# Performance work log

Measured on AMD Instinct MI355X. Metric: run time of the kernel, lower is better.

The kernel has to match this reference:

```python
import jax, jax.numpy as jnp
import numpy as np

# module constants (from init_kwargs)
CS, NV, ED = 8, 4, 32          # codebook_size, num_variables, embedding_dim
VIEWS, D, KSZ = 3, 16, 3        # num_input_channels, depth, kernel_size
HW = 14                         # 7 * scale (scale=2)
CSP = 8                         # spatial of conv_shape after three valid 3x3 convs: 14->12->10->8
KSTATES = CS ** NV              # 4096 combinatorial discrete states


def _elu(x):
    return jnp.where(x > 0, x, jnp.expm1(x))


def _conv_t(x, w, b):
    # PyTorch ConvTranspose2d(stride=1, padding=0); w: (Cin, Cout, k, k)
    wf = jnp.flip(w, (2, 3)).transpose(1, 0, 2, 3)  # -> (Cout, Cin, k, k)
    p = w.shape[2] - 1
    y = jax.lax.conv_general_dilated(x, wf, (1, 1), [(p, p), (p, p)],
                                     dimension_numbers=('NCHW', 'OIHW', 'NCHW'))
    return y + b[None, :, None, None]


def setup_inputs() -> dict:
    key = jax.random.key(0)
    ks = jax.random.split(key, 10)
    rn = lambda k, shape, s=1.0: jax.random.normal(k, shape, jnp.float32) * s
    return {
        'x': rn(ks[0], (64, VIEWS, HW, HW)),
        'latent_embedding': rn(ks[1], (NV, CS, ED)),
        'lin_w': rn(ks[2], (VIEWS, ED * NV, 4 * D * CSP * CSP), 0.05),
        'lin_b': rn(ks[3], (VIEWS, 4 * D * CSP * CSP), 0.05),
        'w1': rn(ks[4], (VIEWS, 4 * D, 2 * D, KSZ, KSZ), 0.05),
        'b1': rn(ks[5], (VIEWS, 2 * D), 0.05),
        'w2': rn(ks[6], (VIEWS, 2 * D, D, KSZ, KSZ), 0.05),
        'b2': rn(ks[7], (VIEWS, D), 0.05),
        'w3': rn(ks[8], (VIEWS, D, 1, KSZ, KSZ), 0.05),
        'b3': rn(ks[9], (VIEWS, 1), 0.05),
    }


def reference(x, latent_embedding, lin_w, lin_b, w1, b1, w2, b2, w3, b3):
    # all combinations of codebook indices (itertools.product order): [K, NV]
    all_idcs = jnp.stack(
        jnp.meshgrid(*([jnp.arange(CS)] * NV), indexing='ij'), -1).reshape(-1, NV)
    # gather: z[k, v, :] = latent_embedding[v, all_idcs[k, v], :]
    z = latent_embedding[jnp.arange(NV)[None, :], all_idcs]       # [K, NV, ED]
    zf = z.reshape(KSTATES, NV * ED)                              # 'b n d -> b (n d)'

    def decode(lw, lb, W1, B1, W2, B2, W3, B3):
        h = (zf @ lw + lb).reshape(KSTATES, 4 * D, CSP, CSP)
        h = _elu(_conv_t(h, W1, B1))
        h = _elu(_conv_t(h, W2, B2))
        h = _conv_t(h, W3, B3)
        return h[:, 0]                                            # [K, HW, HW]

    m = jax.vmap(decode)(lin_w, lin_b, w1, b1, w2, b2, w3, b3)    # [views, K, HW, HW]
    m = jnp.transpose(m, (1, 0, 2, 3))                            # [K, views, HW, HW]

    # obs_logits = -0.5 * sum_{h,w} (m[None] - x[:, None])**2, computed without
    # materializing the [B, K, views, HW, HW] broadcast tensor
    m2 = jnp.sum(m * m, axis=(-2, -1))                            # [K, views]
    x2 = jnp.sum(x * x, axis=(-2, -1))                            # [B, views]
    cross = jnp.einsum('kvhw,bvhw->bkv', m, x)                    # [B, K, views]
    return -0.5 * (m2[None] + x2[:, None] - 2.0 * cross)          # [B, K, views]
```

## Files before the change

### kernel.cpp

```cpp
#include <hip/hip_runtime.h>
#include <cstddef>


typedef __attribute__((ext_vector_type(4))) float f32x4;
typedef _Float16 half8v __attribute__((ext_vector_type(8)));
typedef _Float16 half4v __attribute__((ext_vector_type(4)));
typedef _Float16 half2v __attribute__((ext_vector_type(2)));

static __device__ __forceinline__ float elu(float s) {
    float e = __expf(s) - 1.0f;
    return s > 0.f ? s : e;
}
static __device__ __forceinline__ float dot2acc(int hpair, int wpair, float acc) {
#if __has_builtin(__builtin_amdgcn_fdot2)
    return __builtin_amdgcn_fdot2(__builtin_bit_cast(half2v, hpair),
                                  __builtin_bit_cast(half2v, wpair), acc, false);
#else
    half2v h = __builtin_bit_cast(half2v, hpair);
    half2v w = __builtin_bit_cast(half2v, wpair);
    acc = fmaf((float)h.x, (float)w.x, acc);
    return fmaf((float)h.y, (float)w.y, acc);
#endif
}
static __device__ __forceinline__ int sh2addr(int c, int r) {
    return c * 392 + r * 24 + (((r >> 2) & 3) << 3);
}

__global__ __launch_bounds__(320) void prep_kernel(const float* __restrict__ x,
                                                   const float* __restrict__ le,
                                                   const float* __restrict__ lin_w,
                                                   const float* __restrict__ lin_b,
                                                   const float* __restrict__ w1,
                                                   const float* __restrict__ b1,
                                                   const float* __restrict__ w2,
                                                   float* __restrict__ Qa,
                                                   float* __restrict__ Qb,
                                                   float* __restrict__ x2,
                                                   short* __restrict__ xB,
                                                   short* __restrict__ Wf) {
    int bid = blockIdx.x;
    int t = threadIdx.x;
    if (bid >= 198) {
        int pid = bid - 198;
        int v = pid % 3, part = pid / 3;
        if (part < 4) {
            int nb = part;
            short* xBv = xB + v * 14336 + nb * 3584;
            for (int idx = t; idx < 3584; idx += 320) {
                int j = idx & 7, lane = (idx >> 3) & 63, s = idx >> 9;
                int px = s * 32 + ((lane >> 4) << 3) + j;
                int b  = nb * 16 + (lane & 15);
                float val = (px < 196) ? x[(b * 3 + v) * 196 + px] : 0.f;
                _Float16 h = (_Float16)val;
                xBv[idx] = __builtin_bit_cast(short, h);
            }
        } else if (part == 4) {
            int w = t >> 6, lane = t & 63;
            for (int b = w; b < 64; b += 5) {
                const float* xp = x + (b * 3 + v) * 196;
                float s = 0.f;
                for (int px = lane; px < 196; px += 64) s = fmaf(xp[px], xp[px], s);
#pragma unroll
                for (int off = 32; off; off >>= 1) s += __shfl_down(s, off, 64);
                if (lane == 0) x2[v * 64 + b] = s;
            }
        } else if (t < 64) {
            int lane = t;
            const float* w2v = w2 + v * 32 * 16 * 9;
            int co = lane & 15;
            int cibase = (lane >> 4) * 8;
#pragma unroll
            for (int tap = 0; tap < 9; ++tap)
#pragma unroll
                for (int j = 0; j < 8; ++j) {
                    _Float16 h = (_Float16)w2v[((cibase + j) * 16 + co) * 9 + tap];
                    Wf[(((v * 9 + tap) * 64 + lane) << 3) + j] = __builtin_bit_cast(short, h);
                }
        }
        return;
    }
    __shared__ float sPt[64 * 144];
    __shared__ float sW[16 * 32 * 9];
    int row = bid % 33;
    int v   = (bid / 33) % 3;
    int z   = bid / 99;

    float pacc[16];
    if (t < 256) {
        if (row < 32) {
            int vp = row >> 3;
            const float* base0 = lin_w + (size_t)v * 524288 + (size_t)vp * 32 * 4096 + t;
            const float* lep = le + row * 32;
#pragma unroll
            for (int j = 0; j < 16; ++j) pacc[j] = 0.f;
            for (int e = 0; e < 32; ++e) {
                float lv = lep[e];
                const float* bp = base0 + e * 4096;
#pragma unroll
                for (int j = 0; j < 16; ++j)
                    pacc[j] = fmaf(lv, bp[j * 256], pacc[j]);
            }
        } else {
            const float* bp = lin_b + v * 4096 + t;
#pragma unroll
            for (int j = 0; j < 16; ++j) pacc[j] = bp[j * 256];
        }
    }
    float4* zp = (float4*)sPt;
    for (int i = t; i < 2304; i += 320) zp[i] = float4{0.f, 0.f, 0.f, 0.f};
    __syncthreads();
    if (t < 256) {
#pragma unroll
        for (int j = 0; j < 16; ++j) {
            int i = t + j * 256;
            int ci = i >> 6, r = i & 63, y = r >> 3, xx = r & 7;
            sPt[ci * 144 + (xx + 2) * 12 + (y + 2)] = pacc[j];
        }
    }
    const float* w1v = w1 + (size_t)v * 64 * 32 * 9;
    int co = t / 10, ox = t % 10;
    float acc[10];
#pragma unroll
    for (int i = 0; i < 10; ++i) acc[i] = 0.f;

    for (int c0 = z * 2; c0 < z * 2 + 2; ++c0) {
        __syncthreads();
        for (int i = t; i < 4608; i += 320) sW[i] = w1v[c0 * 4608 + i];
        __syncthreads();
#pragma unroll 2
        for (int ci = 0; ci < 16; ++ci) {
            const float* xp = sPt + (c0 * 16 + ci) * 144;
            const float* wp = sW + (ci * 32 + co) * 9;
            float wv[9];
#pragma unroll
            for (int j = 0; j < 9; ++j) wv[j] = wp[j];
#pragma unroll
            for (int b = 0; b < 3; ++b) {
                const float* colp = xp + (ox + 2 - b) * 12;
                float4 c0v = *(const float4*)(colp);
                float4 c1v = *(const float4*)(colp + 4);
                float4 c2v = *(const float4*)(colp + 8);
                float cv[12] = {c0v.x, c0v.y, c0v.z, c0v.w,
                                c1v.x, c1v.y, c1v.z, c1v.w,
                                c2v.x, c2v.y, c2v.z, c2v.w};
#pragma unroll
                for (int a = 0; a < 3; ++a) {
                    float wgt = wv[a * 3 + b];
#pragma unroll
                    for (int oy = 0; oy < 10; ++oy)
                        acc[oy] = fmaf(cv[oy + 2 - a], wgt, acc[oy]);
                }
            }
        }
    }
    float bb = (z == 0 && row == 32) ? b1[v * 32 + co] : 0.f;
    float* dst = (z == 0 ? Qa : Qb) + (size_t)v * 105600 + row * 3200;
#pragma unroll
    for (int oy = 0; oy < 10; ++oy)
        dst[(ox * 10 + oy) * 32 + co] = acc[oy] + bb;
}

__global__ __launch_bounds__(256) void pair_kernel(const float* __restrict__ Qa,
                                                   const float* __restrict__ Qb,
                                                   float* __restrict__ Q01,
                                                   float* __restrict__ Q23b) {
    int p = blockIdx.x;
    int half = blockIdx.y;
    int v = blockIdx.z;
    const float4* basea = (const float4*)(Qa + (size_t)v * 105600);
    const float4* baseb = (const float4*)(Qb + (size_t)v * 105600);
    if (half == 0) {
        const float4* ra = basea + (p >> 3) * 800;
        const float4* rb = baseb + (p >> 3) * 800;
        const float4* rc = basea + (8 + (p & 7)) * 800;
        const float4* rd = baseb + (8 + (p & 7)) * 800;
        float4* dst = (float4*)(Q01 + (size_t)v * 204800 + p * 3200);
        for (int i = threadIdx.x; i < 800; i += 256) {
            float4 a = ra[i], b = rb[i], c = rc[i], d = rd[i];
            dst[i] = float4{a.x + b.x + c.x + d.x, a.y + b.y + c.y + d.y,
                            a.z + b.z + c.z + d.z, a.w + b.w + c.w + d.w};
        }
    } else {
        const float4* ra = basea + (16 + (p >> 3)) * 800;
        const float4* rb = baseb + (16 + (p >> 3)) * 800;
        const float4* rc = basea + (24 + (p & 7)) * 800;
        const float4* rd = baseb + (24 + (p & 7)) * 800;
        const float4* re = basea + 32 * 800;
        const float4* rf = baseb + 32 * 800;
        float4* dst = (float4*)(Q23b + (size_t)v * 204800 + p * 3200);
        for (int i = threadIdx.x; i < 800; i += 256) {
            float4 a = ra[i], b = rb[i], c = rc[i], d = rd[i], e = re[i], f = rf[i];
            dst[i] = float4{a.x + b.x + c.x + d.x + e.x + f.x,
                            a.y + b.y + c.y + d.y + e.y + f.y,
                            a.z + b.z + c.z + d.z + e.z + f.z,
                            a.w + b.w + c.w + d.w + e.w + f.w};
        }
    }
}

__global__ __launch_bounds__(256) void fused_kernel(const float* __restrict__ Q01,
                                                    const float* __restrict__ Q23b,
                                                    const short* __restrict__ Wf,
                                                    const float* __restrict__ b2,
                                                    const float* __restrict__ w3,
                                                    const float* __restrict__ b3,
                                                    short* __restrict__ Mh,
                                                    float* __restrict__ m2g) {
    __shared__ alignas(16) short sH1[196 * 40];
    __shared__ alignas(16) short sH2[6280];
    __shared__ int sW3p[72];
    __shared__ float sM2;
    int k = blockIdx.x;
    int v = blockIdx.y;
    int t = threadIdx.x;
    int lane = t & 63;
    int g = lane >> 4;

    half8v bfrag[9];
#pragma unroll
    for (int tap = 0; tap < 9; ++tap)
        bfrag[tap] = *(const half8v*)(const void*)(Wf + (((v * 9 + tap) * 64 + lane) << 3));
    float bias2 = b2[v * 16 + (lane & 15)];

    if (t == 0) sM2 = 0.f;
    for (int pix = t; pix < 196; pix += 256) {
        int c = pix / 14, r = pix % 14;
        if (c < 2 || c >= 12 || r < 2 || r >= 12) {
            int4* z = (int4*)(sH1 + pix * 40);
            z[0] = int4{0,0,0,0}; z[1] = int4{0,0,0,0};
            z[2] = int4{0,0,0,0}; z[3] = int4{0,0,0,0};
        }
    }
    {
        int pix = t;
        int c = pix >> 4, r = pix & 15;
        if (c < 2 || c >= 14 || r < 2 || r >= 14) {
            int4* z = (int4*)(sH2 + sh2addr(c, r));
            z[0] = int4{0,0,0,0}; z[1] = int4{0,0,0,0};
        }
    }
    if (t < 72) {
        int tap = t / 8, j = t % 8;
        half2v p = {(_Float16)w3[v * 144 + (2 * j) * 9 + tap],
                    (_Float16)w3[v * 144 + (2 * j + 1) * 9 + tap]};
        sW3p[t] = __builtin_bit_cast(int, p);
    }

    {
        const float4* qa = (const float4*)(Q01  + ((size_t)v * 64 + (k >> 6)) * 3200);
        const float4* qb = (const float4*)(Q23b + ((size_t)v * 64 + (k & 63)) * 3200);
        int ci4 = (t & 7) * 4;
        int pix = t >> 3;
        int cx = pix / 10, ry = pix % 10;
        for (int i = t; i < 800; i += 256) {
            float4 a = qa[i], b = qb[i];
            half4v o = {(_Float16)elu(a.x + b.x), (_Float16)elu(a.y + b.y),
                        (_Float16)elu(a.z + b.z), (_Float16)elu(a.w + b.w)};
            *(half4v*)(void*)(sH1 + ((cx + 2) * 14 + (ry + 2)) * 40 + ci4) = o;
            cx += 3; ry += 2;
            if (ry >= 10) { ry -= 10; ++cx; }
        }
    }
    __syncthreads();

    {
        int w = t >> 6;
        for (int tile = w; tile < 9; tile += 4) {
            int m = tile * 16 + (lane & 15);
            int cx2 = m / 12, ry2 = m % 12;
            const short* basemin = sH1 + (cx2 * 14 + ry2) * 40 + g * 8;
            f32x4 acc0 = {bias2, bias2, bias2, bias2};
            f32x4 acc1 = {0.f, 0.f, 0.f, 0.f};
#pragma unroll
            for (int a = 0; a < 3; ++a)
#pragma unroll
                for (int b = 0; b < 3; ++b) {
                    half8v af = *(const half8v*)(const void*)(basemin + ((2 - b) * 14 + (2 - a)) * 40);
                    int idx = a * 3 + b;
                    if (idx & 1)
                        acc1 = __builtin_amdgcn_mfma_f32_16x16x32_f16(af, bfrag[idx], acc1, 0, 0, 0);
                    else
                        acc0 = __builtin_amdgcn_mfma_f32_16x16x32_f16(af, bfrag[idx], acc0, 0, 0, 0);
                }
            int p0 = tile * 16 + g * 4;
            int cxp = p0 / 12, ryp = p0 % 12;
            int co = lane & 15;
#pragma unroll
            for (int r = 0; r < 4; ++r) {
                _Float16 h = (_Float16)elu(acc0[r] + acc1[r]);
                sH2[sh2addr(cxp + 2, ryp + 2) + co] = __builtin_bit_cast(short, h);
                ++ryp; if (ryp == 12) { ryp = 0; ++cxp; }
            }
        }
    }
    __syncthreads();

    {
        float mval = 0.f;
        if (t < 196) {
            float bias3 = b3[v];
            int ry3 = t / 14, cx3 = t % 14;
            float a0 = bias3, a1 = 0.f, a2 = 0.f, a3 = 0.f;
#pragma unroll
            for (int a = 0; a < 3; ++a)
#pragma unroll
                for (int b = 0; b < 3; ++b) {
                    const short* base = sH2 + sh2addr(cx3 + 2 - b, ry3 + 2 - a);
                    int4 lo = *(const int4*)(const void*)(base);
                    int4 hi = *(const int4*)(const void*)(base + 8);
                    const int* wp = sW3p + (a * 3 + b) * 8;
                    a0 = dot2acc(lo.x, wp[0], a0);
                    a1 = dot2acc(lo.y, wp[1], a1);
                    a2 = dot2acc(lo.z, wp[2], a2);
                    a3 = dot2acc(lo.w, wp[3], a3);
                    a0 = dot2acc(hi.x, wp[4], a0);
                    a1 = dot2acc(hi.y, wp[5], a1);
                    a2 = dot2acc(hi.z, wp[6], a2);
                    a3 = dot2acc(hi.w, wp[7], a3);
                }
            mval = (a0 + a1) + (a2 + a3);
        }
        if (t < 224) {
            _Float16 h = (_Float16)mval;
            Mh[((size_t)v * 4096 + k) * 224 + t] = __builtin_bit_cast(short, h);
        }
        float sq = mval * mval;
#pragma unroll
        for (int off = 32; off; off >>= 1) sq += __shfl_down(sq, off, 64);
        if (lane == 0) atomicAdd(&sM2, sq);
        __syncthreads();
        if (t == 0) m2g[(size_t)v * 4096 + k] = sM2;
    }
}

__global__ __launch_bounds__(256) void gemm_final_kernel(const short* __restrict__ Mh,
                                                         const short* __restrict__ xB,
                                                         const float* __restrict__ m2g,
                                                         const float* __restrict__ x2g,
                                                         float* __restrict__ out) {
    __shared__ float sC[3 * 64 * 17];
    __shared__ float sM2t[48];
    int t = threadIdx.x, lane = t & 63, nb = t >> 6;
    int k0 = blockIdx.x * 16;
    if (t < 48) {
        int v = t % 3, kk = t / 3;
        sM2t[kk * 3 + v] = m2g[(size_t)v * 4096 + k0 + kk];
    }
    int mrow = lane & 15;
    int g = lane >> 4;
#pragma unroll
    for (int v = 0; v < 3; ++v) {
        f32x4 acc = {0.f, 0.f, 0.f, 0.f};
        const short* abase = Mh + ((size_t)v * 4096 + k0 + mrow) * 224 + g * 8;
        const short* bbase = xB + (((v * 4 + nb) * 7) * 64 + lane) * 8;
#pragma unroll
        for (int s = 0; s < 7; ++s) {
            half8v af = *(const half8v*)(const void*)(abase + s * 32);
            half8v bf = *(const half8v*)(const void*)(bbase + s * 512);
            acc = __builtin_amdgcn_mfma_f32_16x16x32_f16(af, bf, acc, 0, 0, 0);
        }
        int b = nb * 16 + mrow;
#pragma unroll
        for (int r = 0; r < 4; ++r)
            sC[(v * 64 + b) * 17 + g * 4 + r] = acc[r];
    }
    __syncthreads();
    int b = t >> 2, q = t & 3;
    float x2v0 = x2g[b], x2v1 = x2g[64 + b], x2v2 = x2g[128 + b];
    float buf[12];
#pragma unroll
    for (int i = 0; i < 4; ++i) {
        int kk = q * 4 + i;
        buf[i * 3 + 0] = sC[(0 * 64 + b) * 17 + kk] - 0.5f * (sM2t[kk * 3 + 0] + x2v0);
        buf[i * 3 + 1] = sC[(1 * 64 + b) * 17 + kk] - 0.5f * (sM2t[kk * 3 + 1] + x2v1);
        buf[i * 3 + 2] = sC[(2 * 64 + b) * 17 + kk] - 0.5f * (sM2t[kk * 3 + 2] + x2v2);
    }
    float* dst = out + ((size_t)b * 4096 + k0) * 3 + q * 12;
    *(float4*)(dst)     = float4{buf[0], buf[1], buf[2],  buf[3]};
    *(float4*)(dst + 4) = float4{buf[4], buf[5], buf[6],  buf[7]};
    *(float4*)(dst + 8) = float4{buf[8], buf[9], buf[10], buf[11]};
}

extern "C" void kernel_launch(void* const* d_in, const int* in_sizes, int n_in,
                              void* d_out, int out_size, void* d_ws, size_t ws_size,
                              hipStream_t stream) {
    const float* x     = (const float*)d_in[0];
    const float* le    = (const float*)d_in[1];
    const float* lin_w = (const float*)d_in[2];
    const float* lin_b = (const float*)d_in[3];
    const float* w1    = (const float*)d_in[4];
    const float* b1    = (const float*)d_in[5];
    const float* w2    = (const float*)d_in[6];
    const float* b2    = (const float*)d_in[7];
    const float* w3    = (const float*)d_in[8];
    const float* b3    = (const float*)d_in[9];
    float* out = (float*)d_out;

    float* ws = (float*)d_ws;
    float* x2g  = ws;
    short* xB   = (short*)(ws + 192);
    short* Wf   = (short*)(ws + 21760);
    float* Qa   = ws + 28736;
    float* Qb   = ws + 345536;
    float* Q01  = ws + 662336;
    float* Q23b = ws + 1276736;
    short* Mh   = (short*)(ws + 1891136);
    float* m2g  = ws + 3267392;

    prep_kernel<<<216, 320, 0, stream>>>(x, le, lin_w, lin_b, w1, b1, w2,
                                         Qa, Qb, x2g, xB, Wf);
    pair_kernel<<<dim3(64, 2, 3), 256, 0, stream>>>(Qa, Qb, Q01, Q23b);
    fused_kernel<<<dim3(4096, 3), 256, 0, stream>>>(Q01, Q23b, Wf, b2, w3, b3, Mh, m2g);
    gemm_final_kernel<<<256, 256, 0, stream>>>(Mh, xB, m2g, x2g, out);
}
```

Before: 180.6 us.

## Drop pair kernel, merge conv1 partials via atomics, process two states per block

Removes the pair-sum kernel. The two z-halves of the first transposed conv now accumulate into one Q buffer with atomicAdd after a memset. The fused kernel handles two codebook states per block: it sums the three shared per-variable partials once, adds the fourth per state, and keeps two H2 buffers. The lin_w and w1 loads also become float4-vectorized. This trades an extra kernel and its intermediate buffers for atomics, a memset, more LDS per block, and half as many blocks.

```diff
diff --git a/kernel.cpp b/kernel.cpp
--- a/kernel.cpp
+++ b/kernel.cpp
@@ -33,8 +33,7 @@
                                                    const float* __restrict__ w1,
                                                    const float* __restrict__ b1,
                                                    const float* __restrict__ w2,
-                                                   float* __restrict__ Qa,
-                                                   float* __restrict__ Qb,
+                                                   float* __restrict__ Q,
                                                    float* __restrict__ x2,
                                                    short* __restrict__ xB,
                                                    short* __restrict__ Wf) {
@@ -85,39 +84,52 @@
     int v   = (bid / 33) % 3;
     int z   = bid / 99;
 
-    float pacc[16];
+    float pj[16];
     if (t < 256) {
         if (row < 32) {
             int vp = row >> 3;
-            const float* base0 = lin_w + (size_t)v * 524288 + (size_t)vp * 32 * 4096 + t;
+            const float* base0 = lin_w + (size_t)v * 524288 + (size_t)vp * 131072 + t * 16;
             const float* lep = le + row * 32;
-#pragma unroll
-            for (int j = 0; j < 16; ++j) pacc[j] = 0.f;
+            f32x4 a0 = {0,0,0,0}, a1 = {0,0,0,0}, a2 = {0,0,0,0}, a3 = {0,0,0,0};
             for (int e = 0; e < 32; ++e) {
                 float lv = lep[e];
-                const float* bp = base0 + e * 4096;
-#pragma unroll
-                for (int j = 0; j < 16; ++j)
-                    pacc[j] = fmaf(lv, bp[j * 256], pacc[j]);
+                const float4* bp = (const float4*)(base0 + e * 4096);
+                float4 b0 = bp[0], b1v_ = bp[1], b2v_ = bp[2], b3v_ = bp[3];
+                a0[0] = fmaf(lv, b0.x, a0[0]);  a0[1] = fmaf(lv, b0.y, a0[1]);
+                a0[2] = fmaf(lv, b0.z, a0[2]);  a0[3] = fmaf(lv, b0.w, a0[3]);
+                a1[0] = fmaf(lv, b1v_.x, a1[0]); a1[1] = fmaf(lv, b1v_.y, a1[1]);
+                a1[2] = fmaf(lv, b1v_.z, a1[2]); a1[3] = fmaf(lv, b1v_.w, a1[3]);
+                a2[0] = fmaf(lv, b2v_.x, a2[0]); a2[1] = fmaf(lv, b2v_.y, a2[1]);
+                a2[2] = fmaf(lv, b2v_.z, a2[2]); a2[3] = fmaf(lv, b2v_.w, a2[3]);
+                a3[0] = fmaf(lv, b3v_.x, a3[0]); a3[1] = fmaf(lv, b3v_.y, a3[1]);
+                a3[2] = fmaf(lv, b3v_.z, a3[2]); a3[3] = fmaf(lv, b3v_.w, a3[3]);
+            }
+#pragma unroll
+            for (int j = 0; j < 4; ++j) {
+                pj[j] = a0[j]; pj[4 + j] = a1[j]; pj[8 + j] = a2[j]; pj[12 + j] = a3[j];
             }
         } else {
-            const float* bp = lin_b + v * 4096 + t;
-#pragma unroll
-            for (int j = 0; j < 16; ++j) pacc[j] = bp[j * 256];
+            const float4* bp = (const float4*)(lin_b + v * 4096 + t * 16);
+#pragma unroll
+            for (int j = 0; j < 4; ++j) {
+                float4 b = bp[j];
+                pj[4 * j] = b.x; pj[4 * j + 1] = b.y; pj[4 * j + 2] = b.z; pj[4 * j + 3] = b.w;
+            }
         }
     }
     float4* zp = (float4*)sPt;
     for (int i = t; i < 2304; i += 320) zp[i] = float4{0.f, 0.f, 0.f, 0.f};
     __syncthreads();
     if (t < 256) {
+        int ci = t >> 2;
 #pragma unroll
         for (int j = 0; j < 16; ++j) {
-            int i = t + j * 256;
-            int ci = i >> 6, r = i & 63, y = r >> 3, xx = r & 7;
-            sPt[ci * 144 + (xx + 2) * 12 + (y + 2)] = pacc[j];
-        }
-    }
-    const float* w1v = w1 + (size_t)v * 64 * 32 * 9;
+            int r = (t & 3) * 16 + j;
+            int y = r >> 3, xx = r & 7;
+            sPt[ci * 144 + (xx + 2) * 12 + (y + 2)] = pj[j];
+        }
+    }
+    const float* w1v = w1 + (size_t)v * 18432;
     int co = t / 10, ox = t % 10;
     float acc[10];
 #pragma unroll
@@ -125,7 +137,8 @@
 
     for (int c0 = z * 2; c0 < z * 2 + 2; ++c0) {
         __syncthreads();
-        for (int i = t; i < 4608; i += 320) sW[i] = w1v[c0 * 4608 + i];
+        const float4* wsrc = (const float4*)(w1v + c0 * 4608);
+        for (int i = t; i < 1152; i += 320) ((float4*)sW)[i] = wsrc[i];
         __syncthreads();
 #pragma unroll 2
         for (int ci = 0; ci < 16; ++ci) {
@@ -154,64 +167,29 @@
         }
     }
     float bb = (z == 0 && row == 32) ? b1[v * 32 + co] : 0.f;
-    float* dst = (z == 0 ? Qa : Qb) + (size_t)v * 105600 + row * 3200;
+    float* dst = Q + (size_t)v * 105600 + row * 3200;
 #pragma unroll
     for (int oy = 0; oy < 10; ++oy)
-        dst[(ox * 10 + oy) * 32 + co] = acc[oy] + bb;
-}
-
-__global__ __launch_bounds__(256) void pair_kernel(const float* __restrict__ Qa,
-                                                   const float* __restrict__ Qb,
-                                                   float* __restrict__ Q01,
-                                                   float* __restrict__ Q23b) {
-    int p = blockIdx.x;
-    int half = blockIdx.y;
-    int v = blockIdx.z;
-    const float4* basea = (const float4*)(Qa + (size_t)v * 105600);
-    const float4* baseb = (const float4*)(Qb + (size_t)v * 105600);
-    if (half == 0) {
-        const float4* ra = basea + (p >> 3) * 800;
-        const float4* rb = baseb + (p >> 3) * 800;
-        const float4* rc = basea + (8 + (p & 7)) * 800;
-        const float4* rd = baseb + (8 + (p & 7)) * 800;
-        float4* dst = (float4*)(Q01 + (size_t)v * 204800 + p * 3200);
-        for (int i = threadIdx.x; i < 800; i += 256) {
-            float4 a = ra[i], b = rb[i], c = rc[i], d = rd[i];
-            dst[i] = float4{a.x + b.x + c.x + d.x, a.y + b.y + c.y + d.y,
-                            a.z + b.z + c.z + d.z, a.w + b.w + c.w + d.w};
-        }
-    } else {
-        const float4* ra = basea + (16 + (p >> 3)) * 800;
-        const float4* rb = baseb + (16 + (p >> 3)) * 800;
-        const float4* rc = basea + (24 + (p & 7)) * 800;
-        const float4* rd = baseb + (24 + (p & 7)) * 800;
-        const float4* re = basea + 32 * 800;
-        const float4* rf = baseb + 32 * 800;
-        float4* dst = (float4*)(Q23b + (size_t)v * 204800 + p * 3200);
-        for (int i = threadIdx.x; i < 800; i += 256) {
-            float4 a = ra[i], b = rb[i], c = rc[i], d = rd[i], e = re[i], f = rf[i];
-            dst[i] = float4{a.x + b.x + c.x + d.x + e.x + f.x,
-                            a.y + b.y + c.y + d.y + e.y + f.y,
-                            a.z + b.z + c.z + d.z + e.z + f.z,
-                            a.w + b.w + c.w + d.w + e.w + f.w};
-        }
-    }
-}
-
-__global__ __launch_bounds__(256) void fused_kernel(const float* __restrict__ Q01,
-                                                    const float* __restrict__ Q23b,
+        atomicAdd(&dst[(ox * 10 + oy) * 32 + co], acc[oy] + bb);
+}
+
+__global__ __launch_bounds__(256) void fused_kernel(const float* __restrict__ Q,
                                                     const short* __restrict__ Wf,
                                                     const float* __restrict__ b2,
                                                     const float* __restrict__ w3,
                                                     const float* __restrict__ b3,
                                                     short* __restrict__ Mh,
                                                     float* __restrict__ m2g) {
-    __shared__ alignas(16) short sH1[196 * 40];
-    __shared__ alignas(16) short sH2[6280];
+    __shared__ alignas(16) short sMem[20520];
     __shared__ int sW3p[72];
-    __shared__ float sM2;
-    int k = blockIdx.x;
-    int v = blockIdx.y;
+    __shared__ float sM2[2];
+    short* sH1  = sMem;
+    short* sH2a = sMem + 7840;
+    short* sB   = sMem + 14120;
+    float* sQf  = (float*)(void*)sB;
+
+    int k0 = blockIdx.x * 2;
+    int v  = blockIdx.y;
     int t = threadIdx.x;
     int lane = t & 63;
     int g = lane >> 4;
@@ -221,8 +199,7 @@
     for (int tap = 0; tap < 9; ++tap)
         bfrag[tap] = *(const half8v*)(const void*)(Wf + (((v * 9 + tap) * 64 + lane) << 3));
     float bias2 = b2[v * 16 + (lane & 15)];
-
-    if (t == 0) sM2 = 0.f;
+    if (t < 2) sM2[t] = 0.f;
     for (int pix = t; pix < 196; pix += 256) {
         int c = pix / 14, r = pix % 14;
         if (c < 2 || c >= 12 || r < 2 || r >= 12) {
@@ -232,10 +209,9 @@
         }
     }
     {
-        int pix = t;
-        int c = pix >> 4, r = pix & 15;
+        int c = t >> 4, r = t & 15;
         if (c < 2 || c >= 14 || r < 2 || r >= 14) {
-            int4* z = (int4*)(sH2 + sh2addr(c, r));
+            int4* z = (int4*)(sH2a + sh2addr(c, r));
             z[0] = int4{0,0,0,0}; z[1] = int4{0,0,0,0};
         }
     }
@@ -246,56 +222,84 @@
         sW3p[t] = __builtin_bit_cast(int, p);
     }
 
+    const float* Qv = Q + (size_t)v * 105600;
     {
-        const float4* qa = (const float4*)(Q01  + ((size_t)v * 64 + (k >> 6)) * 3200);
-        const float4* qb = (const float4*)(Q23b + ((size_t)v * 64 + (k & 63)) * 3200);
-        int ci4 = (t & 7) * 4;
-        int pix = t >> 3;
-        int cx = pix / 10, ry = pix % 10;
+        const float4* q0 = (const float4*)(Qv + ((k0 >> 9) & 7) * 3200);
+        const float4* q1 = (const float4*)(Qv + (8  + ((k0 >> 6) & 7)) * 3200);
+        const float4* q2 = (const float4*)(Qv + (16 + ((k0 >> 3) & 7)) * 3200);
+        const float4* qb = (const float4*)(Qv + 32 * 3200);
+        float4* dstq = (float4*)sQf;
         for (int i = t; i < 800; i += 256) {
-            float4 a = qa[i], b = qb[i];
-            half4v o = {(_Float16)elu(a.x + b.x), (_Float16)elu(a.y + b.y),
-                        (_Float16)elu(a.z + b.z), (_Float16)elu(a.w + b.w)};
-            *(half4v*)(void*)(sH1 + ((cx + 2) * 14 + (ry + 2)) * 40 + ci4) = o;
-            cx += 3; ry += 2;
-            if (ry >= 10) { ry -= 10; ++cx; }
+            float4 a = q0[i], b = q1[i], c = q2[i], d = qb[i];
+            dstq[i] = float4{a.x + b.x + c.x + d.x, a.y + b.y + c.y + d.y,
+                             a.z + b.z + c.z + d.z, a.w + b.w + c.w + d.w};
         }
     }
     __syncthreads();
 
-    {
-        int w = t >> 6;
-        for (int tile = w; tile < 9; tile += 4) {
-            int m = tile * 16 + (lane & 15);
-            int cx2 = m / 12, ry2 = m % 12;
-            const short* basemin = sH1 + (cx2 * 14 + ry2) * 40 + g * 8;
-            f32x4 acc0 = {bias2, bias2, bias2, bias2};
-            f32x4 acc1 = {0.f, 0.f, 0.f, 0.f};
-#pragma unroll
-            for (int a = 0; a < 3; ++a)
-#pragma unroll
-                for (int b = 0; b < 3; ++b) {
-                    half8v af = *(const half8v*)(const void*)(basemin + ((2 - b) * 14 + (2 - a)) * 40);
-                    int idx = a * 3 + b;
-                    if (idx & 1)
-                        acc1 = __builtin_amdgcn_mfma_f32_16x16x32_f16(af, bfrag[idx], acc1, 0, 0, 0);
-                    else
-                        acc0 = __builtin_amdgcn_mfma_f32_16x16x32_f16(af, bfrag[idx], acc0, 0, 0, 0);
+#pragma unroll
+    for (int s = 0; s < 2; ++s) {
+        int k = k0 + s;
+        {
+            const float4* q3 = (const float4*)(Qv + (24 + (k & 7)) * 3200);
+            const float4* qs = (const float4*)sQf;
+            int ci4 = (t & 7) * 4;
+            int pix = t >> 3;
+            int cx = pix / 10, ry = pix % 10;
+            for (int i = t; i < 800; i += 256) {
+                float4 a = qs[i], b = q3[i];
+                half4v o = {(_Float16)elu(a.x + b.x), (_Float16)elu(a.y + b.y),
+                            (_Float16)elu(a.z + b.z), (_Float16)elu(a.w + b.w)};
+                *(half4v*)(void*)(sH1 + ((cx + 2) * 14 + (ry + 2)) * 40 + ci4) = o;
+                cx += 3; ry += 2;
+                if (ry >= 10) { ry -= 10; ++cx; }
+            }
+        }
+        __syncthreads();
+        {
+            short* sH2s = s == 0 ? sH2a : sB;
+            if (s == 1) {
+                int c = t >> 4, r = t & 15;
+                if (c < 2 || c >= 14 || r < 2 || r >= 14) {
+                    int4* z = (int4*)(sH2s + sh2addr(c, r));
+                    z[0] = int4{0,0,0,0}; z[1] = int4{0,0,0,0};
                 }
-            int p0 = tile * 16 + g * 4;
-            int cxp = p0 / 12, ryp = p0 % 12;
-            int co = lane & 15;
-#pragma unroll
-            for (int r = 0; r < 4; ++r) {
-                _Float16 h = (_Float16)elu(acc0[r] + acc1[r]);
-                sH2[sh2addr(cxp + 2, ryp + 2) + co] = __builtin_bit_cast(short, h);
-                ++ryp; if (ryp == 12) { ryp = 0; ++cxp; }
-            }
-        }
-    }
-    __syncthreads();
-
-    {
+            }
+            int w = t >> 6;
+            for (int tile = w; tile < 9; tile += 4) {
+                int m = tile * 16 + (lane & 15);
+                int cx2 = m / 12, ry2 = m % 12;
+                const short* basemin = sH1 + (cx2 * 14 + ry2) * 40 + g * 8;
+                f32x4 acc0 = {bias2, bias2, bias2, bias2};
+                f32x4 acc1 = {0.f, 0.f, 0.f, 0.f};
+#pragma unroll
+                for (int a = 0; a < 3; ++a)
+#pragma unroll
+                    for (int b = 0; b < 3; ++b) {
+                        half8v af = *(const half8v*)(const void*)(basemin + ((2 - b) * 14 + (2 - a)) * 40);
+                        int idx = a * 3 + b;
+                        if (idx & 1)
+                            acc1 = __builtin_amdgcn_mfma_f32_16x16x32_f16(af, bfrag[idx], acc1, 0, 0, 0);
+                        else
+                            acc0 = __builtin_amdgcn_mfma_f32_16x16x32_f16(af, bfrag[idx], acc0, 0, 0, 0);
+                    }
+                int p0 = tile * 16 + g * 4;
+                int cxp = p0 / 12, ryp = p0 % 12;
+                int co = lane & 15;
+#pragma unroll
+                for (int r = 0; r < 4; ++r) {
+                    _Float16 h = (_Float16)elu(acc0[r] + acc1[r]);
+                    sH2s[sh2addr(cxp + 2, ryp + 2) + co] = __builtin_bit_cast(short, h);
+                    ++ryp; if (ryp == 12) { ryp = 0; ++cxp; }
+                }
+            }
+        }
+        __syncthreads();
+    }
+
+#pragma unroll
+    for (int s = 0; s < 2; ++s) {
+        const short* sH2s = s == 0 ? sH2a : sB;
         float mval = 0.f;
         if (t < 196) {
             float bias3 = b3[v];
@@ -305,7 +309,7 @@
             for (int a = 0; a < 3; ++a)
 #pragma unroll
                 for (int b = 0; b < 3; ++b) {
-                    const short* base = sH2 + sh2addr(cx3 + 2 - b, ry3 + 2 - a);
+                    const short* base = sH2s + sh2addr(cx3 + 2 - b, ry3 + 2 - a);
                     int4 lo = *(const int4*)(const void*)(base);
                     int4 hi = *(const int4*)(const void*)(base + 8);
                     const int* wp = sW3p + (a * 3 + b) * 8;
@@ -322,15 +326,15 @@
         }
         if (t < 224) {
             _Float16 h = (_Float16)mval;
-            Mh[((size_t)v * 4096 + k) * 224 + t] = __builtin_bit_cast(short, h);
+            Mh[((size_t)v * 4096 + k0 + s) * 224 + t] = __builtin_bit_cast(short, h);
         }
         float sq = mval * mval;
 #pragma unroll
         for (int off = 32; off; off >>= 1) sq += __shfl_down(sq, off, 64);
-        if (lane == 0) atomicAdd(&sM2, sq);
-        __syncthreads();
-        if (t == 0) m2g[(size_t)v * 4096 + k] = sM2;
-    }
+        if (lane == 0) atomicAdd(&sM2[s], sq);
+    }
+    __syncthreads();
+    if (t < 2) m2g[(size_t)v * 4096 + k0 + t] = sM2[t];
 }
 
 __global__ __launch_bounds__(256) void gemm_final_kernel(const short* __restrict__ Mh,
@@ -400,16 +404,13 @@
     float* x2g  = ws;
     short* xB   = (short*)(ws + 192);
     short* Wf   = (short*)(ws + 21760);
-    float* Qa   = ws + 28736;
-    float* Qb   = ws + 345536;
-    float* Q01  = ws + 662336;
-    float* Q23b = ws + 1276736;
-    short* Mh   = (short*)(ws + 1891136);
-    float* m2g  = ws + 3267392;
-
+    float* Q    = ws + 28736;
+    short* Mh   = (short*)(ws + 345536);
+    float* m2g  = ws + 1721792;
+
+    hipMemsetAsync(Q, 0, 316800 * sizeof(float), stream);
     prep_kernel<<<216, 320, 0, stream>>>(x, le, lin_w, lin_b, w1, b1, w2,
-                                         Qa, Qb, x2g, xB, Wf);
-    pair_kernel<<<dim3(64, 2, 3), 256, 0, stream>>>(Qa, Qb, Q01, Q23b);
-    fused_kernel<<<dim3(4096, 3), 256, 0, stream>>>(Q01, Q23b, Wf, b2, w3, b3, Mh, m2g);
+                                         Q, x2g, xB, Wf);
+    fused_kernel<<<dim3(2048, 3), 256, 0, stream>>>(Q, Wf, b2, w3, b3, Mh, m2g);
     gemm_final_kernel<<<256, 256, 0, stream>>>(Mh, xB, m2g, x2g, out);
 }
```

After: 189.6 us. 1.05x slower.
